# Kernel optimization log

Measured on AMD Instinct MI355X. Metric: run time of the kernel, lower is better.

## Reference

```python
import jax, jax.numpy as jnp
import numpy as np

DIM, H, HD, S, K = 2560, 40, 64, 64, 4  # dim, n_heads, head_dim, state_dim, conv kernel
EPS = 1e-5


def _layer_norm(x, g, b):
    m = jnp.mean(x, axis=-1, keepdims=True)
    v = jnp.mean((x - m) ** 2, axis=-1, keepdims=True)
    return (x - m) * jax.lax.rsqrt(v + EPS) * g + b


def setup_inputs() -> dict:
    key = jax.random.key(0)
    ks = jax.random.split(key, 10)
    w = lambda k, shape: jax.random.normal(k, shape, jnp.float32) * 0.02
    return {
        "x": jax.random.normal(ks[0], (2, 2048, DIM), jnp.float32),
        "W_r": w(ks[1], (DIM, DIM)),
        "W_k": w(ks[2], (DIM, DIM)),
        "W_v": w(ks[3], (DIM, DIM)),
        "W_g": w(ks[4], (DIM, DIM)),
        "W_xproj": w(ks[5], (H * 3 * S, DIM)),
        "W_dt": w(ks[6], (DIM, H * S)),
        "b_dt": jnp.ones((DIM,), jnp.float32),  # dt_proj bias init to 1.0
        "conv_w": w(ks[7], (DIM, 1, K)),  # depthwise conv (out=DIM, in/groups=1, k)
        "ln1_g": jnp.ones((DIM,), jnp.float32),
        "ln1_b": jnp.zeros((DIM,), jnp.float32),
        "ln2_g": jnp.ones((DIM,), jnp.float32),
        "ln2_b": jnp.zeros((DIM,), jnp.float32),
        "W_out": w(ks[8], (DIM, DIM)),
    }


def reference(x, W_r, W_k, W_v, W_g, W_xproj, W_dt, b_dt, conv_w,
              ln1_g, ln1_b, ln2_g, ln2_b, W_out):
    B, L, D = x.shape
    # causal depthwise conv: torch Conv1d(pad=3)[:, :L] == left-pad by K-1
    xc = jax.lax.conv_general_dilated(
        x.transpose(0, 2, 1), conv_w, window_strides=(1,), padding=[(K - 1, 0)],
        feature_group_count=D, dimension_numbers=("NCH", "OIH", "NCH"),
    ).transpose(0, 2, 1)
    x = _layer_norm(x + xc, ln1_g, ln1_b)

    proj = (x @ W_xproj.T).reshape(B, L, H, 3 * S)
    dt_raw, B_vec, C_vec = jnp.split(proj, 3, axis=-1)  # each (B,L,H,S)
    dt = jax.nn.softplus(dt_raw.reshape(B, L, H * S) @ W_dt.T + b_dt)
    w = jnp.exp(-dt).reshape(B, L, H, S)

    r = jax.nn.sigmoid(x @ W_r.T).reshape(B, L, H, HD)
    k = (x @ W_k.T).reshape(B, L, H, HD)
    v = (x @ W_v.T).reshape(B, L, H, HD)
    g = jax.nn.sigmoid(x @ W_g.T).reshape(B, L, H, HD)
    kv = k * v  # (B,L,H,HD)

    def step(state, inp):
        w_t, B_t, C_t, kv_t, r_t, g_t = inp
        # state: (B,H,S,HD); decay per state row, rank-1 B ⊗ (k*v) update
        state = w_t[..., None] * state + B_t[..., None] * kv_t[:, :, None, :]
        y = jnp.einsum("bhsd,bhs->bhd", state, C_t)
        return state, r_t * y * g_t

    seq = tuple(jnp.moveaxis(a, 1, 0) for a in (w, B_vec, C_vec, kv, r, g))
    state0 = jnp.zeros((B, H, S, HD), x.dtype)
    final_state, outs = jax.lax.scan(step, state0, seq)  # outs: (L,B,H,HD)
    out = jnp.moveaxis(outs, 0, 1).reshape(B, L, D)
    out = _layer_norm(x + out @ W_out.T, ln2_g, ln2_b)
    return out, final_state
```

## Files before the change

### kernel.cpp

```cpp
#include <hip/hip_runtime.h>
#include <cstddef>
#include <cstdint>

#define DIM 2560
#define NH 40
#define HDD 64
#define SD 64
#define KC 4
#define BB 2
#define LL 2048
#define MTOT (BB*LL)
#define NPROJ (NH*3*SD)
#define NC 16
#define CH (LL/NC)
#define BH (BB*NH)

typedef unsigned short u16;
typedef __attribute__((ext_vector_type(8))) short bf16x8;
typedef __attribute__((ext_vector_type(4))) float f32x4;

__device__ inline float bf2f(u16 u) { return __uint_as_float(((unsigned)u) << 16); }
__device__ inline float bflo(unsigned u) { return __uint_as_float(u << 16); }
__device__ inline float bfhi(unsigned u) { return __uint_as_float(u & 0xffff0000u); }
__device__ inline u16 f2bf(float f) {
  unsigned x = __float_as_uint(f);
  unsigned r = (x + 0x7fffu + ((x >> 16) & 1u)) >> 16;
  return (u16)r;
}

__device__ inline void gload16(const void* g, void* lds) {
  __builtin_amdgcn_global_load_lds(
      (const __attribute__((address_space(1))) void*)g,
      (__attribute__((address_space(3))) void*)(uint32_t)(size_t)lds,
      16, 0, 0);
}

__global__ __launch_bounds__(256) void cvt_kernel(
    const float* __restrict__ src, u16* __restrict__ dst, int n4) {
  int i = blockIdx.x * 256 + threadIdx.x;
  int stride = gridDim.x * 256;
  for (; i < n4; i += stride) {
    float4 v = *(const float4*)(src + (size_t)i * 4);
    ushort4 o;
    o.x = f2bf(v.x); o.y = f2bf(v.y); o.z = f2bf(v.z); o.w = f2bf(v.w);
    *(ushort4*)(dst + (size_t)i * 4) = o;
  }
}

__global__ __launch_bounds__(256) void fill_kernel(float* p, int n, float v) {
  int i = blockIdx.x * 256 + threadIdx.x;
  if (i < n) p[i] = v;
}

__device__ inline void block_reduce2(float& sum, float& sq, float* red) {
  #pragma unroll
  for (int off = 32; off; off >>= 1) {
    sum += __shfl_down(sum, off, 64);
    sq  += __shfl_down(sq,  off, 64);
  }
  int wid = threadIdx.x >> 6, lane = threadIdx.x & 63;
  if (lane == 0) { red[wid*2] = sum; red[wid*2+1] = sq; }
  __syncthreads();
  sum = red[0] + red[2] + red[4] + red[6];
  sq  = red[1] + red[3] + red[5] + red[7];
}

__global__ __launch_bounds__(256) void conv_ln1_kernel(
    const float* __restrict__ x, const float* __restrict__ cw,
    const float* __restrict__ g1, const float* __restrict__ b1,
    u16* __restrict__ x1) {
  __shared__ float red[8];
  int bl = blockIdx.x;
  int l  = bl & (LL - 1);
  int t  = threadIdx.x;
  const float* xr = x + (size_t)bl * DIM;
  float vals[10];
  float sum = 0.f, sq = 0.f;
  #pragma unroll
  for (int i = 0; i < 10; ++i) {
    int d = t + 256 * i;
    float acc = xr[d];
    #pragma unroll
    for (int j = 0; j < KC; ++j) {
      int ll = l - (KC - 1) + j;
      if (ll >= 0) acc += x[(size_t)(bl - l + ll) * DIM + d] * cw[d * KC + j];
    }
    vals[i] = acc; sum += acc; sq += acc * acc;
  }
  block_reduce2(sum, sq, red);
  float mean = sum * (1.f / DIM);
  float var  = sq * (1.f / DIM) - mean * mean;
  float rstd = rsqrtf(var + 1e-5f);
  u16* orow = x1 + (size_t)bl * DIM;
  #pragma unroll
  for (int i = 0; i < 10; ++i) {
    int d = t + 256 * i;
    orow[d] = f2bf((vals[i] - mean) * rstd * g1[d] + b1[d]);
  }
}

__global__ __launch_bounds__(256) void ln2_kernel(
    const u16* __restrict__ x1, const u16* __restrict__ y2,
    const float* __restrict__ g2, const float* __restrict__ b2,
    float* __restrict__ out) {
  __shared__ float red[8];
  int bl = blockIdx.x;
  int t  = threadIdx.x;
  const u16* ar = x1 + (size_t)bl * DIM;
  const u16* br = y2 + (size_t)bl * DIM;
  float vals[10];
  float sum = 0.f, sq = 0.f;
  #pragma unroll
  for (int i = 0; i < 10; ++i) {
    int d = t + 256 * i;
    float v = bf2f(ar[d]) + bf2f(br[d]);
    vals[i] = v; sum += v; sq += v * v;
  }
  block_reduce2(sum, sq, red);
  float mean = sum * (1.f / DIM);
  float var  = sq * (1.f / DIM) - mean * mean;
  float rstd = rsqrtf(var + 1e-5f);
  float* orow = out + (size_t)bl * DIM;
  #pragma unroll
  for (int i = 0; i < 10; ++i) {
    int d = t + 256 * i;
    orow[d] = (vals[i] - mean) * rstd * g2[d] + b2[d];
  }
}

template<int EPI, bool REMAP>
__global__ __launch_bounds__(256) void gemm_mfma(
    const u16* __restrict__ A, int lda,
    const u16* __restrict__ Wb,
    const float* __restrict__ bias,
    u16* __restrict__ C1, int ldc,
    int K) {
  __shared__ u16 As[128 * 32];
  __shared__ u16 Bs[128 * 32];
  int t = threadIdx.x;
  int w = t >> 6, l = t & 63;
  int wr = w >> 1, wc = w & 1;
  int m0 = blockIdx.y * 128;
  int n0 = blockIdx.x * 128;

  f32x4 acc[4][4];
  #pragma unroll
  for (int i = 0; i < 4; ++i)
    #pragma unroll
    for (int j = 0; j < 4; ++j)
      acc[i][j] = (f32x4){0.f, 0.f, 0.f, 0.f};

  int srow = 32 * w + (l >> 2);
  int scol = (l & 3) * 8;
  const u16* gA = A  + (size_t)(m0 + srow) * lda + scol;
  const u16* gB = Wb + (size_t)(n0 + srow) * K   + scol;
  u16* ldsA = As + (32 * w) * 32;
  u16* ldsB = Bs + (32 * w) * 32;

  int fr = l & 15;
  int kc = (l >> 4) * 8;
  const u16* rA = As + (size_t)(wr * 64 + fr) * 32 + kc;
  const u16* rB = Bs + (size_t)(wc * 64 + fr) * 32 + kc;

  for (int k0 = 0; k0 < K; k0 += 32) {
    gload16(gA + k0, ldsA);
    gload16(gA + (size_t)16 * lda + k0, ldsA + 16 * 32);
    gload16(gB + k0, ldsB);
    gload16(gB + (size_t)16 * K + k0, ldsB + 16 * 32);
    __syncthreads();
    bf16x8 a[4], b[4];
    #pragma unroll
    for (int i = 0; i < 4; ++i) a[i] = *(const bf16x8*)(rA + i * 16 * 32);
    #pragma unroll
    for (int j = 0; j < 4; ++j) b[j] = *(const bf16x8*)(rB + j * 16 * 32);
    #pragma unroll
    for (int i = 0; i < 4; ++i)
      #pragma unroll
      for (int j = 0; j < 4; ++j)
        acc[i][j] = __builtin_amdgcn_mfma_f32_16x16x32_bf16(a[i], b[j], acc[i][j], 0, 0, 0);
    __syncthreads();
  }

  int crow = (l >> 4) * 4;
  int ccol = l & 15;
  #pragma unroll
  for (int j = 0; j < 4; ++j) {
    int col = n0 + wc * 64 + j * 16 + ccol;
    int colr = col;
    if (REMAP) {
      int h = col / 192, r3 = col % 192;
      colr = (r3 / 64) * 2560 + h * 64 + (r3 & 63);
    }
    float bv = (EPI == 2) ? bias[col] : 0.f;
    #pragma unroll
    for (int i = 0; i < 4; ++i) {
      #pragma unroll
      for (int q = 0; q < 4; ++q) {
        int row = m0 + wr * 64 + i * 16 + crow + q;
        float v = acc[i][j][q];
        if constexpr (EPI == 1) v = 1.f / (1.f + expf(-v));
        if constexpr (EPI == 2) v = 1.f / (1.f + expf(v + bv));
        size_t idx = (size_t)row * ldc + colr;
        if constexpr (EPI == 5) v *= bf2f(C1[idx]);
        C1[idx] = f2bf(v);
      }
    }
  }
}

__global__ __launch_bounds__(128) void scan_local_kernel(
    const u16* __restrict__ wdec, const u16* __restrict__ proj,
    const u16* __restrict__ kvb, u16* __restrict__ yout,
    float* __restrict__ Sbuf, float* __restrict__ Pbuf) {
  int bx = blockIdx.x;
  int bh = bx / NC, c = bx % NC;
  int b = bh / NH, h = bh % NH;
  int wv = threadIdx.x >> 6;
  int lane = threadIdx.x & 63;
  int sg = lane >> 3, dd = lane & 7;
  int s0 = sg * 8;
  int d0 = wv * 32 + dd * 4;
  int l0 = c * CH;

  const u16* fw = wdec + ((size_t)(b * LL + l0)) * DIM + h * 64 + s0;
  const u16* fB = proj + ((size_t)(b * LL + l0)) * NPROJ + 2560 + h * 64 + s0;
  const u16* fC = fB + 2560;
  const u16* fk = kvb + ((size_t)(b * LL + l0)) * DIM + h * 64 + d0;
  u16* py = yout + ((size_t)(b * LL + l0)) * NPROJ + h * 64 + d0;

  float st[8][4];
  float pc[8];
  #pragma unroll
  for (int i = 0; i < 8; ++i) {
    pc[i] = 1.f;
    #pragma unroll
    for (int j = 0; j < 4; ++j) st[i][j] = 0.f;
  }

#define P1_DECL(n) uint4 wS##n, BS##n, CS##n; uint2 kS##n
#define P1_LOAD(n) do { \
    wS##n = *(const uint4*)fw; BS##n = *(const uint4*)fB; \
    CS##n = *(const uint4*)fC; kS##n = *(const uint2*)fk; \
    fw += DIM; fB += NPROJ; fC += NPROJ; fk += DIM; } while (0)
#define P1_PROC(n) do { \
    float wv8[8], Bv[8], Cv[8], kv4[4], pr[4]; \
    wv8[0]=bflo(wS##n.x); wv8[1]=bfhi(wS##n.x); wv8[2]=bflo(wS##n.y); wv8[3]=bfhi(wS##n.y); \
    wv8[4]=bflo(wS##n.z); wv8[5]=bfhi(wS##n.z); wv8[6]=bflo(wS##n.w); wv8[7]=bfhi(wS##n.w); \
    Bv[0]=bflo(BS##n.x); Bv[1]=bfhi(BS##n.x); Bv[2]=bflo(BS##n.y); Bv[3]=bfhi(BS##n.y); \
    Bv[4]=bflo(BS##n.z); Bv[5]=bfhi(BS##n.z); Bv[6]=bflo(BS##n.w); Bv[7]=bfhi(BS##n.w); \
    Cv[0]=bflo(CS##n.x); Cv[1]=bfhi(CS##n.x); Cv[2]=bflo(CS##n.y); Cv[3]=bfhi(CS##n.y); \
    Cv[4]=bflo(CS##n.z); Cv[5]=bfhi(CS##n.z); Cv[6]=bflo(CS##n.w); Cv[7]=bfhi(CS##n.w); \
    kv4[0]=bflo(kS##n.x); kv4[1]=bfhi(kS##n.x); kv4[2]=bflo(kS##n.y); kv4[3]=bfhi(kS##n.y); \
    pr[0]=0.f; pr[1]=0.f; pr[2]=0.f; pr[3]=0.f; \
    _Pragma("unroll") \
    for (int i = 0; i < 8; ++i) { \
      pc[i] *= wv8[i]; \
      _Pragma("unroll") \
      for (int j = 0; j < 4; ++j) { \
        st[i][j] = fmaf(wv8[i], st[i][j], Bv[i] * kv4[j]); \
        pr[j] = fmaf(st[i][j], Cv[i], pr[j]); } } \
    _Pragma("unroll") \
    for (int j = 0; j < 4; ++j) { \
      pr[j] += __shfl_xor(pr[j], 8, 64); \
      pr[j] += __shfl_xor(pr[j], 16, 64); \
      pr[j] += __shfl_xor(pr[j], 32, 64); } \
    if (lane < 8) { \
      uint2 ov; \
      ov.x = (unsigned)f2bf(pr[0]) | ((unsigned)f2bf(pr[1]) << 16); \
      ov.y = (unsigned)f2bf(pr[2]) | ((unsigned)f2bf(pr[3]) << 16); \
      *(uint2*)py = ov; } \
    py += NPROJ; } while (0)

  P1_DECL(0); P1_DECL(1); P1_DECL(2); P1_DECL(3);
  P1_LOAD(0); P1_LOAD(1); P1_LOAD(2); P1_LOAD(3);
  for (int l = 0; l < CH; l += 4) {
    P1_PROC(0); P1_LOAD(0);
    P1_PROC(1); P1_LOAD(1);
    P1_PROC(2); P1_LOAD(2);
    P1_PROC(3); P1_LOAD(3);
  }
#undef P1_DECL
#undef P1_LOAD
#undef P1_PROC

  float* Sp = Sbuf + (((size_t)c * BH + bh) * 64 + s0) * 64 + d0;
  #pragma unroll
  for (int i = 0; i < 8; ++i) {
    float4 v; v.x = st[i][0]; v.y = st[i][1]; v.z = st[i][2]; v.w = st[i][3];
    *(float4*)(Sp + (size_t)i * 64) = v;
  }
  if (wv == 0 && dd == 0) {
    #pragma unroll
    for (int i = 0; i < 8; ++i)
      Pbuf[((size_t)c * BH + bh) * 64 + s0 + i] = pc[i];
  }
}

__global__ __launch_bounds__(256) void scan_combine_kernel(
    float* __restrict__ Sbuf, const float* __restrict__ Pbuf,
    float* __restrict__ fstate) {
  int bh = blockIdx.x;
  int t = threadIdx.x;
  int s = t >> 2, j0 = (t & 3) * 16;
  float stin[16];
  #pragma unroll
  for (int k = 0; k < 16; ++k) stin[k] = 0.f;
  for (int c = 0; c < NC; ++c) {
    float* Sp = Sbuf + (((size_t)c * BH + bh) * 64 + s) * 64 + j0;
    float Pc = Pbuf[((size_t)c * BH + bh) * 64 + s];
    #pragma unroll
    for (int q = 0; q < 4; ++q) {
      float4 a = *(const float4*)(Sp + q * 4);
      float4 cur;
      cur.x = stin[q*4+0]; cur.y = stin[q*4+1];
      cur.z = stin[q*4+2]; cur.w = stin[q*4+3];
      *(float4*)(Sp + q * 4) = cur;
      stin[q*4+0] = a.x + Pc * stin[q*4+0];
      stin[q*4+1] = a.y + Pc * stin[q*4+1];
      stin[q*4+2] = a.z + Pc * stin[q*4+2];
      stin[q*4+3] = a.w + Pc * stin[q*4+3];
    }
  }
  float* fp = fstate + ((size_t)bh * 64 + s) * 64 + j0;
  #pragma unroll
  for (int q = 0; q < 4; ++q) {
    float4 v;
    v.x = stin[q*4+0]; v.y = stin[q*4+1];
    v.z = stin[q*4+2]; v.w = stin[q*4+3];
    *(float4*)(fp + q * 4) = v;
  }
}

__global__ __launch_bounds__(128) void scan_correct_kernel(
    const u16* __restrict__ wdec, const u16* __restrict__ proj,
    const float* __restrict__ Sbuf, u16* __restrict__ yio) {
  int bx = blockIdx.x;
  int bh = bx / NC, c = bx % NC;
  int b = bh / NH, h = bh % NH;
  int wv = threadIdx.x >> 6;
  int lane = threadIdx.x & 63;
  int sg = lane >> 3, dd = lane & 7;
  int s0 = sg * 8;
  int d0 = wv * 32 + dd * 4;
  int l0 = c * CH;

  const float* Sp = Sbuf + (((size_t)c * BH + bh) * 64 + s0) * 64 + d0;
  float stin[8][4];
  #pragma unroll
  for (int i = 0; i < 8; ++i) {
    float4 v = *(const float4*)(Sp + (size_t)i * 64);
    stin[i][0] = v.x; stin[i][1] = v.y; stin[i][2] = v.z; stin[i][3] = v.w;
  }

  const u16* fw = wdec + ((size_t)(b * LL + l0)) * DIM + h * 64 + s0;
  const u16* fC = proj + ((size_t)(b * LL + l0)) * NPROJ + 5120 + h * 64 + s0;
  const u16* fy = yio  + ((size_t)(b * LL + l0)) * NPROJ + h * 64 + d0;
  u16* py = yio + ((size_t)(b * LL + l0)) * NPROJ + h * 64 + d0;

  float pc[8];
  #pragma unroll
  for (int i = 0; i < 8; ++i) pc[i] = 1.f;

#define P3_DECL(n) uint4 wT##n, CT##n; uint2 yT##n
#define P3_LOAD(n) do { \
    wT##n = *(const uint4*)fw; CT##n = *(const uint4*)fC; \
    yT##n = *(const uint2*)fy; \
    fw += DIM; fC += NPROJ; fy += NPROJ; } while (0)
#define P3_PROC(n) do { \
    float wv8[8], Cv[8], ac[8], pr[4]; \
    wv8[0]=bflo(wT##n.x); wv8[1]=bfhi(wT##n.x); wv8[2]=bflo(wT##n.y); wv8[3]=bfhi(wT##n.y); \
    wv8[4]=bflo(wT##n.z); wv8[5]=bfhi(wT##n.z); wv8[6]=bflo(wT##n.w); wv8[7]=bfhi(wT##n.w); \
    Cv[0]=bflo(CT##n.x); Cv[1]=bfhi(CT##n.x); Cv[2]=bflo(CT##n.y); Cv[3]=bfhi(CT##n.y); \
    Cv[4]=bflo(CT##n.z); Cv[5]=bfhi(CT##n.z); Cv[6]=bflo(CT##n.w); Cv[7]=bfhi(CT##n.w); \
    pr[0]=0.f; pr[1]=0.f; pr[2]=0.f; pr[3]=0.f; \
    _Pragma("unroll") \
    for (int i = 0; i < 8; ++i) { \
      pc[i] *= wv8[i]; ac[i] = pc[i] * Cv[i]; \
      _Pragma("unroll") \
      for (int j = 0; j < 4; ++j) pr[j] = fmaf(ac[i], stin[i][j], pr[j]); } \
    _Pragma("unroll") \
    for (int j = 0; j < 4; ++j) { \
      pr[j] += __shfl_xor(pr[j], 8, 64); \
      pr[j] += __shfl_xor(pr[j], 16, 64); \
      pr[j] += __shfl_xor(pr[j], 32, 64); } \
    if (lane < 8) { \
      float y0 = bflo(yT##n.x) + pr[0]; \
      float y1 = bfhi(yT##n.x) + pr[1]; \
      float y2 = bflo(yT##n.y) + pr[2]; \
      float y3 = bfhi(yT##n.y) + pr[3]; \
      uint2 ov; \
      ov.x = (unsigned)f2bf(y0) | ((unsigned)f2bf(y1) << 16); \
      ov.y = (unsigned)f2bf(y2) | ((unsigned)f2bf(y3) << 16); \
      *(uint2*)py = ov; } \
    py += NPROJ; } while (0)

  P3_DECL(0); P3_DECL(1); P3_DECL(2); P3_DECL(3);
  P3_LOAD(0); P3_LOAD(1); P3_LOAD(2); P3_LOAD(3);
  for (int l = 0; l < CH; l += 4) {
    P3_PROC(0); P3_LOAD(0);
    P3_PROC(1); P3_LOAD(1);
    P3_PROC(2); P3_LOAD(2);
    P3_PROC(3); P3_LOAD(3);
  }
#undef P3_DECL
#undef P3_LOAD
#undef P3_PROC
}

__global__ __launch_bounds__(320) void gate_kernel(
    const u16* __restrict__ proj, const u16* __restrict__ rb,
    const u16* __restrict__ gb, u16* __restrict__ outi) {
  int bl = blockIdx.x, t = threadIdx.x;
  uint4 yv = *(const uint4*)(proj + (size_t)bl * NPROJ + t * 8);
  uint4 rv = *(const uint4*)(rb + (size_t)bl * DIM + t * 8);
  uint4 gv = *(const uint4*)(gb + (size_t)bl * DIM + t * 8);
  unsigned yw[4] = {yv.x, yv.y, yv.z, yv.w};
  unsigned rw[4] = {rv.x, rv.y, rv.z, rv.w};
  unsigned gw[4] = {gv.x, gv.y, gv.z, gv.w};
  u16 res[8];
  #pragma unroll
  for (int i = 0; i < 4; ++i) {
    res[2*i]   = f2bf(bflo(yw[i]) * bflo(rw[i]) * bflo(gw[i]));
    res[2*i+1] = f2bf(bfhi(yw[i]) * bfhi(rw[i]) * bfhi(gw[i]));
  }
  uint4 ov;
  ov.x = (unsigned)res[0] | ((unsigned)res[1] << 16);
  ov.y = (unsigned)res[2] | ((unsigned)res[3] << 16);
  ov.z = (unsigned)res[4] | ((unsigned)res[5] << 16);
  ov.w = (unsigned)res[6] | ((unsigned)res[7] << 16);
  *(uint4*)(outi + (size_t)bl * DIM + t * 8) = ov;
}

extern "C" void kernel_launch(void* const* d_in, const int* in_sizes, int n_in,
                              void* d_out, int out_size, void* d_ws, size_t ws_size,
                              hipStream_t stream) {
  const float* x    = (const float*)d_in[0];
  const float* W_r  = (const float*)d_in[1];
  const float* W_k  = (const float*)d_in[2];
  const float* W_v  = (const float*)d_in[3];
  const float* W_g  = (const float*)d_in[4];
  const float* W_xp = (const float*)d_in[5];
  const float* W_dt = (const float*)d_in[6];
  const float* b_dt = (const float*)d_in[7];
  const float* cw   = (const float*)d_in[8];
  const float* ln1g = (const float*)d_in[9];
  const float* ln1b = (const float*)d_in[10];
  const float* ln2g = (const float*)d_in[11];
  const float* ln2b = (const float*)d_in[12];
  const float* W_o  = (const float*)d_in[13];

  float* out    = (float*)d_out;
  float* fstate = out + (size_t)MTOT * DIM;

  const size_t nBL = (size_t)MTOT * DIM;
  const size_t nPJ = (size_t)MTOT * NPROJ;
  const size_t nWX = (size_t)NPROJ * DIM;
  const size_t needed = (nBL * 5 + nPJ + nWX) * sizeof(u16);
  if (ws_size < needed) {
    fill_kernel<<<(out_size + 255) / 256, 256, 0, stream>>>(out, out_size, 1234.5f);
    return;
  }

  u16* wsp  = (u16*)d_ws;
  u16* x1   = wsp;
  u16* proj = x1 + nBL;
  u16* wdec = proj + nPJ;
  u16* rb   = wdec + nBL;
  u16* gb   = rb + nBL;
  u16* kvb  = gb + nBL;
  u16* wscr = kvb + nBL;
  float* Sbuf = (float*)wscr;
  float* Pbuf = Sbuf + (size_t)NC * BH * 64 * 64;

  const int nDD4 = DIM * DIM / 4;

  conv_ln1_kernel<<<MTOT, 256, 0, stream>>>(x, cw, ln1g, ln1b, x1);

  cvt_kernel<<<2048, 256, 0, stream>>>(W_xp, wscr, NPROJ * DIM / 4);
  gemm_mfma<0,true ><<<dim3(NPROJ/128, MTOT/128), 256, 0, stream>>>(x1, DIM, wscr, nullptr, proj, NPROJ, DIM);

  cvt_kernel<<<2048, 256, 0, stream>>>(W_dt, wscr, nDD4);
  gemm_mfma<2,false><<<dim3(DIM/128, MTOT/128), 256, 0, stream>>>(proj, NPROJ, wscr, b_dt, wdec, DIM, DIM);

  cvt_kernel<<<2048, 256, 0, stream>>>(W_r, wscr, nDD4);
  gemm_mfma<1,false><<<dim3(DIM/128, MTOT/128), 256, 0, stream>>>(x1, DIM, wscr, nullptr, rb, DIM, DIM);

  cvt_kernel<<<2048, 256, 0, stream>>>(W_g, wscr, nDD4);
  gemm_mfma<1,false><<<dim3(DIM/128, MTOT/128), 256, 0, stream>>>(x1, DIM, wscr, nullptr, gb, DIM, DIM);

  cvt_kernel<<<2048, 256, 0, stream>>>(W_k, wscr, nDD4);
  gemm_mfma<0,false><<<dim3(DIM/128, MTOT/128), 256, 0, stream>>>(x1, DIM, wscr, nullptr, kvb, DIM, DIM);

  cvt_kernel<<<2048, 256, 0, stream>>>(W_v, wscr, nDD4);
  gemm_mfma<5,false><<<dim3(DIM/128, MTOT/128), 256, 0, stream>>>(x1, DIM, wscr, nullptr, kvb, DIM, DIM);

  scan_local_kernel<<<BH * NC, 128, 0, stream>>>(wdec, proj, kvb, proj, Sbuf, Pbuf);
  scan_combine_kernel<<<BH, 256, 0, stream>>>(Sbuf, Pbuf, fstate);
  scan_correct_kernel<<<BH * NC, 128, 0, stream>>>(wdec, proj, Sbuf, proj);

  gate_kernel<<<MTOT, 320, 0, stream>>>(proj, rb, gb, kvb);

  cvt_kernel<<<2048, 256, 0, stream>>>(W_o, wscr, nDD4);
  gemm_mfma<0,false><<<dim3(DIM/128, MTOT/128), 256, 0, stream>>>(kvb, DIM, wscr, nullptr, wdec, DIM, DIM);

  ln2_kernel<<<MTOT, 256, 0, stream>>>(x1, wdec, ln2g, ln2b, out);
}
```

Baseline: 1.085 ms.

## Fuse gating into scan correction, widen GEMM K-step, swizzle GEMM block order

The r*g gating is folded into the scan correction kernel, so the separate gate kernel and its full read/write pass disappear. The output GEMM now reads the gated result directly from the proj buffer. The MFMA GEMM loads a 64-wide K slice per barrier pair, halving synchronisation, and remaps block IDs in groups of 8 for better cache locality. Costs are double the LDS use per block and extra r/g loads inside the latency-bound scan loop.

Measured after the change: 1.077 ms. About the same (-0.8%).

```diff
diff --git a/kernel.cpp b/kernel.cpp
--- a/kernel.cpp
+++ b/kernel.cpp
@@ -135,13 +135,19 @@
     const float* __restrict__ bias,
     u16* __restrict__ C1, int ldc,
     int K) {
-  __shared__ u16 As[128 * 32];
-  __shared__ u16 Bs[128 * 32];
+  __shared__ u16 As[2 * 128 * 32];
+  __shared__ u16 Bs[2 * 128 * 32];
   int t = threadIdx.x;
   int w = t >> 6, l = t & 63;
   int wr = w >> 1, wc = w & 1;
-  int m0 = blockIdx.y * 128;
-  int n0 = blockIdx.x * 128;
+
+  int nx  = gridDim.x;
+  int nwg = nx * gridDim.y;
+  int wg  = blockIdx.y * nx + blockIdx.x;
+  int cpx = nwg >> 3;
+  int swz = (wg & 7) * cpx + (wg >> 3);
+  int m0 = (swz / nx) * 128;
+  int n0 = (swz % nx) * 128;
 
   f32x4 acc[4][4];
   #pragma unroll
@@ -150,10 +156,10 @@
     for (int j = 0; j < 4; ++j)
       acc[i][j] = (f32x4){0.f, 0.f, 0.f, 0.f};
 
-  int srow = 32 * w + (l >> 2);
+  int srow = l >> 2;
   int scol = (l & 3) * 8;
-  const u16* gA = A  + (size_t)(m0 + srow) * lda + scol;
-  const u16* gB = Wb + (size_t)(n0 + srow) * K   + scol;
+  const u16* gA = A  + (size_t)(m0 + 32 * w + srow) * lda + scol;
+  const u16* gB = Wb + (size_t)(n0 + 32 * w + srow) * K   + scol;
   u16* ldsA = As + (32 * w) * 32;
   u16* ldsB = Bs + (32 * w) * 32;
 
@@ -162,22 +168,31 @@
   const u16* rA = As + (size_t)(wr * 64 + fr) * 32 + kc;
   const u16* rB = Bs + (size_t)(wc * 64 + fr) * 32 + kc;
 
-  for (int k0 = 0; k0 < K; k0 += 32) {
-    gload16(gA + k0, ldsA);
-    gload16(gA + (size_t)16 * lda + k0, ldsA + 16 * 32);
-    gload16(gB + k0, ldsB);
-    gload16(gB + (size_t)16 * K + k0, ldsB + 16 * 32);
+  for (int k0 = 0; k0 < K; k0 += 64) {
+    #pragma unroll
+    for (int q = 0; q < 4; ++q) {
+      const int ks = q >> 1, rr = q & 1;
+      gload16(gA + (size_t)(rr * 16) * lda + k0 + ks * 32,
+              ldsA + ks * 4096 + rr * 512);
+      gload16(gB + (size_t)(rr * 16) * K + k0 + ks * 32,
+              ldsB + ks * 4096 + rr * 512);
+    }
     __syncthreads();
-    bf16x8 a[4], b[4];
-    #pragma unroll
-    for (int i = 0; i < 4; ++i) a[i] = *(const bf16x8*)(rA + i * 16 * 32);
-    #pragma unroll
-    for (int j = 0; j < 4; ++j) b[j] = *(const bf16x8*)(rB + j * 16 * 32);
-    #pragma unroll
-    for (int i = 0; i < 4; ++i)
+    bf16x8 a[4][2], b[4][2];
+    #pragma unroll
+    for (int i = 0; i < 4; ++i) {
+      a[i][0] = *(const bf16x8*)(rA + i * 512);
+      a[i][1] = *(const bf16x8*)(rA + 4096 + i * 512);
+      b[i][0] = *(const bf16x8*)(rB + i * 512);
+      b[i][1] = *(const bf16x8*)(rB + 4096 + i * 512);
+    }
+    #pragma unroll
+    for (int ks = 0; ks < 2; ++ks)
       #pragma unroll
-      for (int j = 0; j < 4; ++j)
-        acc[i][j] = __builtin_amdgcn_mfma_f32_16x16x32_bf16(a[i], b[j], acc[i][j], 0, 0, 0);
+      for (int i = 0; i < 4; ++i)
+        #pragma unroll
+        for (int j = 0; j < 4; ++j)
+          acc[i][j] = __builtin_amdgcn_mfma_f32_16x16x32_bf16(a[i][ks], b[j][ks], acc[i][j], 0, 0, 0);
     __syncthreads();
   }
 
@@ -333,6 +348,7 @@
 
 __global__ __launch_bounds__(128) void scan_correct_kernel(
     const u16* __restrict__ wdec, const u16* __restrict__ proj,
+    const u16* __restrict__ rb, const u16* __restrict__ gb,
     const float* __restrict__ Sbuf, u16* __restrict__ yio) {
   int bx = blockIdx.x;
   int bh = bx / NC, c = bx % NC;
@@ -355,17 +371,19 @@
   const u16* fw = wdec + ((size_t)(b * LL + l0)) * DIM + h * 64 + s0;
   const u16* fC = proj + ((size_t)(b * LL + l0)) * NPROJ + 5120 + h * 64 + s0;
   const u16* fy = yio  + ((size_t)(b * LL + l0)) * NPROJ + h * 64 + d0;
+  const u16* fr2 = rb + ((size_t)(b * LL + l0)) * DIM + h * 64 + d0;
+  const u16* fg2 = gb + ((size_t)(b * LL + l0)) * DIM + h * 64 + d0;
   u16* py = yio + ((size_t)(b * LL + l0)) * NPROJ + h * 64 + d0;
 
   float pc[8];
   #pragma unroll
   for (int i = 0; i < 8; ++i) pc[i] = 1.f;
 
-#define P3_DECL(n) uint4 wT##n, CT##n; uint2 yT##n
+#define P3_DECL(n) uint4 wT##n, CT##n; uint2 yT##n, rT##n, gT##n
 #define P3_LOAD(n) do { \
     wT##n = *(const uint4*)fw; CT##n = *(const uint4*)fC; \
-    yT##n = *(const uint2*)fy; \
-    fw += DIM; fC += NPROJ; fy += NPROJ; } while (0)
+    yT##n = *(const uint2*)fy; rT##n = *(const uint2*)fr2; gT##n = *(const uint2*)fg2; \
+    fw += DIM; fC += NPROJ; fy += NPROJ; fr2 += DIM; fg2 += DIM; } while (0)
 #define P3_PROC(n) do { \
     float wv8[8], Cv[8], ac[8], pr[4]; \
     wv8[0]=bflo(wT##n.x); wv8[1]=bfhi(wT##n.x); wv8[2]=bflo(wT##n.y); wv8[3]=bfhi(wT##n.y); \
@@ -384,10 +402,10 @@
       pr[j] += __shfl_xor(pr[j], 16, 64); \
       pr[j] += __shfl_xor(pr[j], 32, 64); } \
     if (lane < 8) { \
-      float y0 = bflo(yT##n.x) + pr[0]; \
-      float y1 = bfhi(yT##n.x) + pr[1]; \
-      float y2 = bflo(yT##n.y) + pr[2]; \
-      float y3 = bfhi(yT##n.y) + pr[3]; \
+      float y0 = (bflo(yT##n.x) + pr[0]) * bflo(rT##n.x) * bflo(gT##n.x); \
+      float y1 = (bfhi(yT##n.x) + pr[1]) * bfhi(rT##n.x) * bfhi(gT##n.x); \
+      float y2 = (bflo(yT##n.y) + pr[2]) * bflo(rT##n.y) * bflo(gT##n.y); \
+      float y3 = (bfhi(yT##n.y) + pr[3]) * bfhi(rT##n.y) * bfhi(gT##n.y); \
       uint2 ov; \
       ov.x = (unsigned)f2bf(y0) | ((unsigned)f2bf(y1) << 16); \
       ov.y = (unsigned)f2bf(y2) | ((unsigned)f2bf(y3) << 16); \
@@ -405,30 +423,6 @@
 #undef P3_DECL
 #undef P3_LOAD
 #undef P3_PROC
-}
-
-__global__ __launch_bounds__(320) void gate_kernel(
-    const u16* __restrict__ proj, const u16* __restrict__ rb,
-    const u16* __restrict__ gb, u16* __restrict__ outi) {
-  int bl = blockIdx.x, t = threadIdx.x;
-  uint4 yv = *(const uint4*)(proj + (size_t)bl * NPROJ + t * 8);
-  uint4 rv = *(const uint4*)(rb + (size_t)bl * DIM + t * 8);
-  uint4 gv = *(const uint4*)(gb + (size_t)bl * DIM + t * 8);
-  unsigned yw[4] = {yv.x, yv.y, yv.z, yv.w};
-  unsigned rw[4] = {rv.x, rv.y, rv.z, rv.w};
-  unsigned gw[4] = {gv.x, gv.y, gv.z, gv.w};
-  u16 res[8];
-  #pragma unroll
-  for (int i = 0; i < 4; ++i) {
-    res[2*i]   = f2bf(bflo(yw[i]) * bflo(rw[i]) * bflo(gw[i]));
-    res[2*i+1] = f2bf(bfhi(yw[i]) * bfhi(rw[i]) * bfhi(gw[i]));
-  }
-  uint4 ov;
-  ov.x = (unsigned)res[0] | ((unsigned)res[1] << 16);
-  ov.y = (unsigned)res[2] | ((unsigned)res[3] << 16);
-  ov.z = (unsigned)res[4] | ((unsigned)res[5] << 16);
-  ov.w = (unsigned)res[6] | ((unsigned)res[7] << 16);
-  *(uint4*)(outi + (size_t)bl * DIM + t * 8) = ov;
 }
 
 extern "C" void kernel_launch(void* const* d_in, const int* in_sizes, int n_in,
@@ -496,12 +490,10 @@
 
   scan_local_kernel<<<BH * NC, 128, 0, stream>>>(wdec, proj, kvb, proj, Sbuf, Pbuf);
   scan_combine_kernel<<<BH, 256, 0, stream>>>(Sbuf, Pbuf, fstate);
-  scan_correct_kernel<<<BH * NC, 128, 0, stream>>>(wdec, proj, Sbuf, proj);
-
-  gate_kernel<<<MTOT, 320, 0, stream>>>(proj, rb, gb, kvb);
+  scan_correct_kernel<<<BH * NC, 128, 0, stream>>>(wdec, proj, rb, gb, Sbuf, proj);
 
   cvt_kernel<<<2048, 256, 0, stream>>>(W_o, wscr, nDD4);
-  gemm_mfma<0,false><<<dim3(DIM/128, MTOT/128), 256, 0, stream>>>(kvb, DIM, wscr, nullptr, wdec, DIM, DIM);
+  gemm_mfma<0,false><<<dim3(DIM/128, MTOT/128), 256, 0, stream>>>(proj, NPROJ, wscr, nullptr, wdec, DIM, DIM);
 
   ln2_kernel<<<MTOT, 256, 0, stream>>>(x1, wdec, ln2g, ln2b, out);
 }
```
